# Kernel tuning notes

Hardware: AMD Instinct MI355X
Metric: run time of the kernel (lower is better)

The kernel has to match this reference:

```python
import jax, jax.numpy as jnp
import numpy as np

N, E, D = 50000, 800000, 128
BN_EPS = 1e-5
COORDS_WEIGHT = 1.0


def _p(key, shape, scale=0.05):
    return (jax.random.normal(key, shape, dtype=jnp.float32) * scale)


def setup_inputs() -> dict:
    key = jax.random.key(0)
    ks = jax.random.split(key, 16)
    inp = {
        "h": jax.random.normal(ks[0], (N, D), dtype=jnp.float32),
        "coord": jax.random.normal(ks[1], (N, 3), dtype=jnp.float32),
        "edge_index": jax.random.randint(ks[2], (2, E), 0, N, dtype=jnp.int32),
        # edge_mlp: Linear(2D+1 -> D), BN, ReLU, Linear(D -> D), BN, ReLU
        "e_w1": _p(ks[3], (D, 2 * D + 1)), "e_b1": jnp.zeros((D,), jnp.float32),
        "e_g1": jnp.ones((D,), jnp.float32), "e_be1": jnp.zeros((D,), jnp.float32),
        "e_w2": _p(ks[4], (D, D)), "e_b2": jnp.zeros((D,), jnp.float32),
        "e_g2": jnp.ones((D,), jnp.float32), "e_be2": jnp.zeros((D,), jnp.float32),
        # node_mlp: Linear(D + D -> D), BN, ReLU, Linear(D -> D)
        "n_w1": _p(ks[5], (D, 2 * D)), "n_b1": jnp.zeros((D,), jnp.float32),
        "n_g1": jnp.ones((D,), jnp.float32), "n_be1": jnp.zeros((D,), jnp.float32),
        "n_w2": _p(ks[6], (D, D)), "n_b2": jnp.zeros((D,), jnp.float32),
        # coord_mlp: Linear(D -> D), BN, ReLU, Linear(D -> 1, bias=False, tiny init)
        "c_w1": _p(ks[7], (D, D)), "c_b1": jnp.zeros((D,), jnp.float32),
        "c_g1": jnp.ones((D,), jnp.float32), "c_be1": jnp.zeros((D,), jnp.float32),
        "c_w2": _p(ks[8], (1, D), scale=0.001),
    }
    return inp


def _bn(x, g, b):
    # BatchNorm1d in training mode: biased batch stats over dim 0
    m = jnp.mean(x, axis=0)
    v = jnp.var(x, axis=0)
    return (x - m) * jax.lax.rsqrt(v + BN_EPS) * g + b


def _segment_mean(data, seg, num_segments):
    s = jax.ops.segment_sum(data, seg, num_segments=num_segments)
    c = jax.ops.segment_sum(jnp.ones((data.shape[0], 1), data.dtype), seg,
                            num_segments=num_segments)
    return s / jnp.maximum(c, 1.0)


def reference(h, coord, edge_index,
              e_w1, e_b1, e_g1, e_be1, e_w2, e_b2, e_g2, e_be2,
              n_w1, n_b1, n_g1, n_be1, n_w2, n_b2,
              c_w1, c_b1, c_g1, c_be1, c_w2):
    row, col = edge_index[0], edge_index[1]
    # coord2radial
    coord_diff = coord[row] - coord[col]                      # [E,3]
    radial = jnp.sum(coord_diff ** 2, axis=1, keepdims=True)  # [E,1]
    # edge_model
    e_in = jnp.concatenate([h[row], h[col], radial], axis=1)  # [E, 2D+1]
    x = jax.nn.relu(_bn(e_in @ e_w1.T + e_b1, e_g1, e_be1))
    edge_feat = jax.nn.relu(_bn(x @ e_w2.T + e_b2, e_g2, e_be2))  # [E,D]
    # coord_model
    y = jax.nn.relu(_bn(edge_feat @ c_w1.T + c_b1, c_g1, c_be1))
    scale = y @ c_w2.T                                        # [E,1]
    trans = jnp.clip(coord_diff * scale, -100.0, 100.0)
    coord_out = coord + _segment_mean(trans, row, coord.shape[0]) * COORDS_WEIGHT
    # node_model
    agg = _segment_mean(edge_feat, row, h.shape[0])           # [N,D]
    n_in = jnp.concatenate([h, agg], axis=1)                  # [N,2D]
    z = jax.nn.relu(_bn(n_in @ n_w1.T + n_b1, n_g1, n_be1))
    h_out = h + (z @ n_w2.T + n_b2)                           # recurrent residual
    return (h_out, coord_out)
```

## Files before the change

kernel.cpp:

```cpp
#include <hip/hip_runtime.h>

#define Nn 50000
#define En 800000
#define NSLOT 64

typedef __attribute__((ext_vector_type(8))) short short8;
typedef __attribute__((ext_vector_type(4))) float f32x4;

union U8 { uint4 u4; unsigned short us[8]; short8 s8; };

static __device__ __forceinline__ float bf2f(unsigned int lo16) {
  return __uint_as_float(lo16 << 16);
}
static __device__ __forceinline__ unsigned short f2bf(float f) {
  unsigned int x = __float_as_uint(f);
  return (unsigned short)((x + 0x7FFFu + ((x >> 16) & 1u)) >> 16);
}


__global__ __launch_bounds__(256) void k_prep_h(const float* __restrict__ h,
                                                unsigned short* __restrict__ nodeA) {
  int idx = blockIdx.x * 256 + threadIdx.x;
  if (idx >= Nn * 128) return;
  int n = idx >> 7, k = idx & 127;
  nodeA[(size_t)n * 256 + k] = f2bf(h[idx]);
}

__global__ __launch_bounds__(256) void k_prep_w(const float* __restrict__ src,
                                                unsigned short* __restrict__ dst, int Ksrc,
                                                int koff, int kshift, int total) {
  int idx = blockIdx.x * 256 + threadIdx.x;
  if (idx >= total) return;
  int n = idx >> kshift;
  int k = idx & ((1 << kshift) - 1);
  dst[idx] = f2bf(src[n * Ksrc + koff + k]);
}

__global__ void k_wlast(const float* __restrict__ e_w1, float* __restrict__ wlast) {
  int t = threadIdx.x;
  if (t < 128) wlast[t] = e_w1[t * 257 + 256];
}


__global__ __launch_bounds__(256) void k_count(const int* __restrict__ row, int* __restrict__ cnt) {
  int e = blockIdx.x * 256 + threadIdx.x;
  atomicAdd(&cnt[row[e]], 1);
}

__global__ __launch_bounds__(256) void k_fill(const int* __restrict__ row,
                                              const int* __restrict__ col,
                                              int* __restrict__ cursor,
                                              unsigned short* __restrict__ rowS,
                                              unsigned short* __restrict__ colS) {
  int e = blockIdx.x * 256 + threadIdx.x;
  int r = row[e];
  int pos = atomicAdd(&cursor[r], 1);
  rowS[pos] = (unsigned short)r;
  colS[pos] = (unsigned short)col[e];
}

__global__ __launch_bounds__(1024) void k_scan(const int* __restrict__ cnt, int* __restrict__ start,
                                               int* __restrict__ cursor, int n) {
  __shared__ int wsum[16];
  __shared__ int carry;
  int tid = threadIdx.x, lane = tid & 63, wid = tid >> 6;
  if (tid == 0) carry = 0;
  __syncthreads();
  for (int base = 0; base < n; base += 1024) {
    int i = base + tid;
    int v = (i < n) ? cnt[i] : 0;
    int x = v;
#pragma unroll
    for (int d = 1; d < 64; d <<= 1) {
      int y = __shfl_up(x, d, 64);
      if (lane >= d) x += y;
    }
    if (lane == 63) wsum[wid] = x;
    __syncthreads();
    if (wid == 0) {
      int s = (lane < 16) ? wsum[lane] : 0;
#pragma unroll
      for (int d = 1; d < 16; d <<= 1) {
        int y = __shfl_up(s, d, 64);
        if (lane >= d) s += y;
      }
      if (lane < 16) wsum[lane] = s;
    }
    __syncthreads();
    int c0 = carry;
    int waveoff = (wid > 0) ? wsum[wid - 1] : 0;
    int incl = c0 + waveoff + x;
    if (i < n) {
      start[i] = incl - v;
      cursor[i] = incl - v;
    }
    __syncthreads();
    if (tid == 1023) carry = incl;
    __syncthreads();
  }
}


__global__ void k_fin(const float* __restrict__ statS, const float* __restrict__ statQ,
                      const float* __restrict__ g, const float* __restrict__ be, float invR,
                      float* __restrict__ bnS, float* __restrict__ bnSh) {
  int c = threadIdx.x;
  if (c >= 128) return;
  float s = 0.f, q = 0.f;
  for (int k = 0; k < NSLOT; ++k) {
    s += statS[k * 128 + c];
    q += statQ[k * 128 + c];
  }
  float mean = s * invR;
  float var = fmaxf(q * invR - mean * mean, 0.f);
  float rs = rsqrtf(var + 1e-5f);
  float sc = g[c] * rs;
  bnS[c] = sc;
  bnSh[c] = be[c] - mean * sc;
}

template <int KSTEPS, bool BN_A, bool STATS, bool FP32OUT, bool STORE>
__global__ __launch_bounds__(256) void k_gemmW(
    const unsigned short* __restrict__ A, int Astride,
    const unsigned short* __restrict__ W, const float* __restrict__ bias,
    const float* __restrict__ bnS, const float* __restrict__ bnSh,
    unsigned short* __restrict__ outb, float* __restrict__ statS, float* __restrict__ statQ,
    const float* __restrict__ hres, float* __restrict__ outf, int R) {
  constexpr int K = KSTEPS * 32;
  constexpr int WST = K + 8;
  constexpr int SEGS = K / 8;
  __shared__ __align__(16) unsigned short smem[128 * WST];
  __shared__ float ssum[4][128], ssq[4][128];
  int tid = threadIdx.x;
  int w = tid >> 6, lane = tid & 63, m = lane & 15, kq = lane >> 4;
  int rbase = blockIdx.x * 128;
#pragma unroll
  for (int it = 0; it < SEGS / 2; ++it) {
    int idx = it * 256 + tid;
    int n = idx / SEGS, seg = idx % SEGS;
    uint4 v = *(const uint4*)(W + (size_t)n * K + seg * 8);
    *(uint4*)(smem + n * WST + seg * 8) = v;
  }
  __syncthreads();
  int row0 = rbase + w * 32 + m;
  int rc0 = min(row0, R - 1);
  int rc1 = min(row0 + 16, R - 1);
  f32x4 acc[2][8];
#pragma unroll
  for (int rt = 0; rt < 2; ++rt)
#pragma unroll
    for (int c = 0; c < 8; ++c) acc[rt][c] = (f32x4){0.f, 0.f, 0.f, 0.f};
#pragma unroll
  for (int ks = 0; ks < KSTEPS; ++ks) {
    int k0 = ks * 32 + kq * 8;
    U8 ua0, ua1;
    ua0.u4 = *(const uint4*)(A + (size_t)rc0 * Astride + k0);
    ua1.u4 = *(const uint4*)(A + (size_t)rc1 * Astride + k0);
    if (BN_A) {
      const float4* sp = (const float4*)(bnS + k0);
      const float4* hp = (const float4*)(bnSh + k0);
      float4 s0 = sp[0], s1 = sp[1], h0 = hp[0], h1 = hp[1];
      float sv[8] = {s0.x, s0.y, s0.z, s0.w, s1.x, s1.y, s1.z, s1.w};
      float hv[8] = {h0.x, h0.y, h0.z, h0.w, h1.x, h1.y, h1.z, h1.w};
#pragma unroll
      for (int j = 0; j < 8; ++j) {
        ua0.us[j] = f2bf(fmaxf(bf2f(ua0.us[j]) * sv[j] + hv[j], 0.f));
        ua1.us[j] = f2bf(fmaxf(bf2f(ua1.us[j]) * sv[j] + hv[j], 0.f));
      }
    }
#pragma unroll
    for (int c = 0; c < 8; ++c) {
      U8 ub;
      ub.u4 = *(const uint4*)(smem + (c * 16 + m) * WST + k0);
      acc[0][c] = __builtin_amdgcn_mfma_f32_16x16x32_bf16(ua0.s8, ub.s8, acc[0][c], 0, 0, 0);
      acc[1][c] = __builtin_amdgcn_mfma_f32_16x16x32_bf16(ua1.s8, ub.s8, acc[1][c], 0, 0, 0);
    }
  }
  if constexpr (FP32OUT) {
#pragma unroll
    for (int rt = 0; rt < 2; ++rt)
#pragma unroll
      for (int c = 0; c < 8; ++c) {
        int n = c * 16 + m;
        float bn_ = bias[n];
#pragma unroll
        for (int j = 0; j < 4; ++j) {
          int rr = rbase + w * 32 + rt * 16 + kq * 4 + j;
          if (rr < R) {
            size_t o = (size_t)rr * 128 + n;
            outf[o] = acc[rt][c][j] + bn_ + hres[o];
          }
        }
      }
  } else {
    if constexpr (STORE) __syncthreads();
    unsigned short* tile = smem;
#pragma unroll
    for (int c = 0; c < 8; ++c) {
      int n = c * 16 + m;
      float bn_ = bias ? bias[n] : 0.f;
      float s = 0.f, q = 0.f;
#pragma unroll
      for (int rt = 0; rt < 2; ++rt)
#pragma unroll
        for (int j = 0; j < 4; ++j) {
          int lr = w * 32 + rt * 16 + kq * 4 + j;
          float v = acc[rt][c][j] + bn_;
          if (STORE) tile[lr * 136 + n] = f2bf(v);
          if (STATS) {
            float sv = (rbase + lr < R) ? v : 0.f;
            s += sv;
            q = fmaf(sv, sv, q);
          }
        }
      if (STATS) {
        s += __shfl_xor(s, 16, 64); s += __shfl_xor(s, 32, 64);
        q += __shfl_xor(q, 16, 64); q += __shfl_xor(q, 32, 64);
        if (kq == 0) { ssum[w][n] = s; ssq[w][n] = q; }
      }
    }
    if constexpr (STORE) {
      __syncthreads();
      const uint4* tl = (const uint4*)tile;
#pragma unroll
      for (int u = 0; u < 8; ++u) {
        int idx = u * 256 + tid;
        int rr = idx >> 4, seg = idx & 15;
        if (rbase + rr < R)
          *(uint4*)(outb + (size_t)(rbase + rr) * 128 + seg * 8) = tl[rr * 17 + seg];
      }
    }
    if (STATS) {
      __syncthreads();
      if (tid < 128) {
        float s = ssum[0][tid] + ssum[1][tid] + ssum[2][tid] + ssum[3][tid];
        float q = ssq[0][tid] + ssq[1][tid] + ssq[2][tid] + ssq[3][tid];
        int slot = blockIdx.x & (NSLOT - 1);
        atomicAdd(&statS[slot * 128 + tid], s);
        atomicAdd(&statQ[slot * 128 + tid], q);
      }
    }
  }
}

__global__ __launch_bounds__(256) void k_stats1(
    const unsigned short* __restrict__ hWr, const unsigned short* __restrict__ hWc,
    const float* __restrict__ coord, const unsigned short* __restrict__ rowS,
    const unsigned short* __restrict__ colS, const float* __restrict__ wlast,
    float* __restrict__ radS, float* __restrict__ statS, float* __restrict__ statQ,
    int per_wave) {
  int tid = threadIdx.x, lane = tid & 63;
  int wid = blockIdx.x * 4 + (tid >> 6);
  int e0 = wid * per_wave;
  int e1 = min(e0 + per_wave, En);
  int c2 = lane * 2;
  float wl0 = wlast[c2], wl1 = wlast[c2 + 1];
  float s0 = 0.f, s1 = 0.f, q0 = 0.f, q1 = 0.f;
  for (int e = e0; e < e1; ++e) {
    int r = rowS[e], c = colS[e];
    float dx = coord[r * 3 + 0] - coord[c * 3 + 0];
    float dy = coord[r * 3 + 1] - coord[c * 3 + 1];
    float dz = coord[r * 3 + 2] - coord[c * 3 + 2];
    float rad = dx * dx + dy * dy + dz * dz;
    if (lane == 0) radS[e] = rad;
    unsigned int ua = *(const unsigned int*)(hWr + (size_t)r * 128 + c2);
    unsigned int ub = *(const unsigned int*)(hWc + (size_t)c * 128 + c2);
    float v0 = bf2f(ua & 0xFFFFu) + bf2f(ub & 0xFFFFu) + rad * wl0;
    float v1 = bf2f(ua >> 16) + bf2f(ub >> 16) + rad * wl1;
    s0 += v0; q0 = fmaf(v0, v0, q0);
    s1 += v1; q1 = fmaf(v1, v1, q1);
  }
  int slot = wid & (NSLOT - 1);
  atomicAdd(&statS[slot * 128 + c2], s0);
  atomicAdd(&statS[slot * 128 + c2 + 1], s1);
  atomicAdd(&statQ[slot * 128 + c2], q0);
  atomicAdd(&statQ[slot * 128 + c2 + 1], q1);
}

__global__ __launch_bounds__(256) void k_egemm2(
    const unsigned short* __restrict__ hWr, const unsigned short* __restrict__ hWc,
    const float* __restrict__ radS, const unsigned short* __restrict__ rowS,
    const unsigned short* __restrict__ colS, const unsigned short* __restrict__ W,
    const float* __restrict__ bias, const float* __restrict__ wlast,
    const float* __restrict__ bnS1, const float* __restrict__ bnSh1,
    unsigned short* __restrict__ outb, float* __restrict__ statS, float* __restrict__ statQ) {
  constexpr int WST = 136;
  __shared__ __align__(16) unsigned short smem[128 * WST];
  __shared__ float ssum[4][128], ssq[4][128];
  int tid = threadIdx.x;
  int w = tid >> 6, lane = tid & 63, m = lane & 15, kq = lane >> 4;
  int rbase = blockIdx.x * 128;
#pragma unroll
  for (int it = 0; it < 8; ++it) {
    int idx = it * 256 + tid;
    int n = idx >> 4, seg = idx & 15;
    uint4 v = *(const uint4*)(W + (size_t)n * 128 + seg * 8);
    *(uint4*)(smem + n * WST + seg * 8) = v;
  }
  int rc0 = rbase + w * 32 + m, rc1 = rc0 + 16;
  int r0 = rowS[rc0], c0 = colS[rc0];
  int r1 = rowS[rc1], c1 = colS[rc1];
  float rad0 = radS[rc0], rad1 = radS[rc1];
  __syncthreads();
  f32x4 acc[2][8];
#pragma unroll
  for (int rt = 0; rt < 2; ++rt)
#pragma unroll
    for (int c = 0; c < 8; ++c) acc[rt][c] = (f32x4){0.f, 0.f, 0.f, 0.f};
#pragma unroll
  for (int ks = 0; ks < 4; ++ks) {
    int k0 = ks * 32 + kq * 8;
    U8 a0r, a0c, a1r, a1c;
    a0r.u4 = *(const uint4*)(hWr + (size_t)r0 * 128 + k0);
    a0c.u4 = *(const uint4*)(hWc + (size_t)c0 * 128 + k0);
    a1r.u4 = *(const uint4*)(hWr + (size_t)r1 * 128 + k0);
    a1c.u4 = *(const uint4*)(hWc + (size_t)c1 * 128 + k0);
    const float4* wp = (const float4*)(wlast + k0);
    const float4* sp = (const float4*)(bnS1 + k0);
    const float4* hp = (const float4*)(bnSh1 + k0);
    float4 w0 = wp[0], w1 = wp[1], sA = sp[0], sB = sp[1], hA = hp[0], hB = hp[1];
    float wv[8] = {w0.x, w0.y, w0.z, w0.w, w1.x, w1.y, w1.z, w1.w};
    float sv[8] = {sA.x, sA.y, sA.z, sA.w, sB.x, sB.y, sB.z, sB.w};
    float hv[8] = {hA.x, hA.y, hA.z, hA.w, hB.x, hB.y, hB.z, hB.w};
    U8 ua0, ua1;
#pragma unroll
    for (int j = 0; j < 8; ++j) {
      float v0 = bf2f(a0r.us[j]) + bf2f(a0c.us[j]) + rad0 * wv[j];
      float v1 = bf2f(a1r.us[j]) + bf2f(a1c.us[j]) + rad1 * wv[j];
      ua0.us[j] = f2bf(fmaxf(v0 * sv[j] + hv[j], 0.f));
      ua1.us[j] = f2bf(fmaxf(v1 * sv[j] + hv[j], 0.f));
    }
#pragma unroll
    for (int c = 0; c < 8; ++c) {
      U8 ub;
      ub.u4 = *(const uint4*)(smem + (c * 16 + m) * WST + k0);
      acc[0][c] = __builtin_amdgcn_mfma_f32_16x16x32_bf16(ua0.s8, ub.s8, acc[0][c], 0, 0, 0);
      acc[1][c] = __builtin_amdgcn_mfma_f32_16x16x32_bf16(ua1.s8, ub.s8, acc[1][c], 0, 0, 0);
    }
  }
  __syncthreads();
  unsigned short* tile = smem;
#pragma unroll
  for (int c = 0; c < 8; ++c) {
    int n = c * 16 + m;
    float bn_ = bias[n];
    float s = 0.f, q = 0.f;
#pragma unroll
    for (int rt = 0; rt < 2; ++rt)
#pragma unroll
      for (int j = 0; j < 4; ++j) {
        int lr = w * 32 + rt * 16 + kq * 4 + j;
        float v = acc[rt][c][j] + bn_;
        tile[lr * 136 + n] = f2bf(v);
        s += v;
        q = fmaf(v, v, q);
      }
    s += __shfl_xor(s, 16, 64); s += __shfl_xor(s, 32, 64);
    q += __shfl_xor(q, 16, 64); q += __shfl_xor(q, 32, 64);
    if (kq == 0) { ssum[w][n] = s; ssq[w][n] = q; }
  }
  __syncthreads();
  const uint4* tl = (const uint4*)tile;
#pragma unroll
  for (int u = 0; u < 8; ++u) {
    int idx = u * 256 + tid;
    int rr = idx >> 4, seg = idx & 15;
    *(uint4*)(outb + (size_t)(rbase + rr) * 128 + seg * 8) = tl[rr * 17 + seg];
  }
  if (tid < 128) {
    float s = ssum[0][tid] + ssum[1][tid] + ssum[2][tid] + ssum[3][tid];
    float q = ssq[0][tid] + ssq[1][tid] + ssq[2][tid] + ssq[3][tid];
    int slot = blockIdx.x & (NSLOT - 1);
    atomicAdd(&statS[slot * 128 + tid], s);
    atomicAdd(&statQ[slot * 128 + tid], q);
  }
}

__global__ __launch_bounds__(256) void k_c1agg(
    const unsigned short* __restrict__ t, const unsigned short* __restrict__ W,
    const float* __restrict__ bias, const float* __restrict__ bnS2,
    const float* __restrict__ bnSh2, const float* __restrict__ bnS3,
    const float* __restrict__ bnSh3, const float* __restrict__ cw2,
    const unsigned short* __restrict__ rowS, float* __restrict__ aggAcc,
    float* __restrict__ scaleE) {
  __shared__ __align__(16) unsigned short smw[128 * 128];
  __shared__ __align__(16) unsigned short ytile[128 * 128];
  int tid = threadIdx.x;
  int w = tid >> 6, lane = tid & 63, m = lane & 15, kq = lane >> 4;
  int rbase = blockIdx.x * 128;
#pragma unroll
  for (int it = 0; it < 8; ++it) {
    int idx = it * 256 + tid;
    int n = idx >> 4, b = idx & 15;
    uint4 v = *(const uint4*)(W + (size_t)n * 128 + b * 8);
    *(uint4*)(smw + n * 128 + ((b ^ (n & 15)) << 3)) = v;
  }
  __syncthreads();
  f32x4 acc[2][8];
#pragma unroll
  for (int rt = 0; rt < 2; ++rt)
#pragma unroll
    for (int c = 0; c < 8; ++c) acc[rt][c] = (f32x4){0.f, 0.f, 0.f, 0.f};
  int r0l = w * 32 + m, r1l = r0l + 16;
#pragma unroll
  for (int ks = 0; ks < 4; ++ks) {
    int k0 = ks * 32 + kq * 8;
    int blk = ks * 4 + kq;
    U8 ua0, ua1;
    ua0.u4 = *(const uint4*)(t + (size_t)(rbase + r0l) * 128 + k0);
    ua1.u4 = *(const uint4*)(t + (size_t)(rbase + r1l) * 128 + k0);
    const float4* sp = (const float4*)(bnS2 + k0);
    const float4* hp = (const float4*)(bnSh2 + k0);
    float4 sA = sp[0], sB = sp[1], hA = hp[0], hB = hp[1];
    float sv[8] = {sA.x, sA.y, sA.z, sA.w, sB.x, sB.y, sB.z, sB.w};
    float hv[8] = {hA.x, hA.y, hA.z, hA.w, hB.x, hB.y, hB.z, hB.w};
#pragma unroll
    for (int j = 0; j < 8; ++j) {
      ua0.us[j] = f2bf(fmaxf(bf2f(ua0.us[j]) * sv[j] + hv[j], 0.f));
      ua1.us[j] = f2bf(fmaxf(bf2f(ua1.us[j]) * sv[j] + hv[j], 0.f));
    }
    *(uint4*)(ytile + r0l * 128 + ((blk ^ m) << 3)) = ua0.u4;
    *(uint4*)(ytile + r1l * 128 + ((blk ^ m) << 3)) = ua1.u4;
#pragma unroll
    for (int c = 0; c < 8; ++c) {
      U8 ub;
      ub.u4 = *(const uint4*)(smw + (c * 16 + m) * 128 + ((blk ^ m) << 3));
      acc[0][c] = __builtin_amdgcn_mfma_f32_16x16x32_bf16(ua0.s8, ub.s8, acc[0][c], 0, 0, 0);
      acc[1][c] = __builtin_amdgcn_mfma_f32_16x16x32_bf16(ua1.s8, ub.s8, acc[1][c], 0, 0, 0);
    }
  }
  float p[2][4] = {{0.f, 0.f, 0.f, 0.f}, {0.f, 0.f, 0.f, 0.f}};
#pragma unroll
  for (int c = 0; c < 8; ++c) {
    int n = c * 16 + m;
    float b1 = bias[n], s3 = bnS3[n], sh3 = bnSh3[n], w2 = cw2[n];
#pragma unroll
    for (int rt = 0; rt < 2; ++rt)
#pragma unroll
      for (int j = 0; j < 4; ++j) {
        float t3v = acc[rt][c][j] + b1;
        p[rt][j] += w2 * fmaxf(t3v * s3 + sh3, 0.f);
      }
  }
#pragma unroll
  for (int rt = 0; rt < 2; ++rt)
#pragma unroll
    for (int j = 0; j < 4; ++j) {
      float v = p[rt][j];
      v += __shfl_xor(v, 1, 64); v += __shfl_xor(v, 2, 64);
      v += __shfl_xor(v, 4, 64); v += __shfl_xor(v, 8, 64);
      if (m == 0) scaleE[rbase + w * 32 + rt * 16 + kq * 4 + j] = v;
    }
  __syncthreads();
  int ch = tid & 127, half = tid >> 7;
  int rlo = half * 64, rhi = rlo + 64;
  int cur = rowS[rbase + rlo];
  float run = 0.f;
  for (int r = rlo; r < rhi; ++r) {
    int nid = rowS[rbase + r];
    if (nid != cur) {
      atomicAdd(&aggAcc[(size_t)cur * 128 + ch], run);
      run = 0.f;
      cur = nid;
    }
    run += bf2f(ytile[r * 128 + (((ch >> 3) ^ (r & 15)) << 3) + (ch & 7)]);
  }
  atomicAdd(&aggAcc[(size_t)cur * 128 + ch], run);
}

__global__ __launch_bounds__(256) void k_aggfin(const float* __restrict__ aggAcc,
                                                const int* __restrict__ cnt,
                                                unsigned short* __restrict__ nodeA) {
  int idx = blockIdx.x * 256 + threadIdx.x;
  if (idx >= Nn * 128) return;
  int n = idx >> 7, ch = idx & 127;
  float inv = 1.f / fmaxf((float)cnt[n], 1.f);
  nodeA[(size_t)n * 256 + 128 + ch] = f2bf(aggAcc[idx] * inv);
}

__global__ __launch_bounds__(256) void k_coord(const float* __restrict__ coord,
                                               const unsigned short* __restrict__ colS,
                                               const int* __restrict__ start,
                                               const int* __restrict__ cnt,
                                               const float* __restrict__ scaleE,
                                               float* __restrict__ cout) {
  int tid = threadIdx.x;
  int lane = tid & 63;
  int n = blockIdx.x * 4 + (tid >> 6);
  if (n >= Nn) return;
  int deg = cnt[n], off = start[n];
  float cx0 = coord[n * 3 + 0], cy0 = coord[n * 3 + 1], cz0 = coord[n * 3 + 2];
  float ax = 0.f, ay = 0.f, az = 0.f;
  for (int j = lane; j < deg; j += 64) {
    int e = off + j;
    int c = colS[e];
    float s = scaleE[e];
    float tx = (cx0 - coord[c * 3 + 0]) * s;
    float ty = (cy0 - coord[c * 3 + 1]) * s;
    float tz = (cz0 - coord[c * 3 + 2]) * s;
    ax += fminf(fmaxf(tx, -100.f), 100.f);
    ay += fminf(fmaxf(ty, -100.f), 100.f);
    az += fminf(fmaxf(tz, -100.f), 100.f);
  }
#pragma unroll
  for (int d = 32; d; d >>= 1) {
    ax += __shfl_xor(ax, d, 64);
    ay += __shfl_xor(ay, d, 64);
    az += __shfl_xor(az, d, 64);
  }
  if (lane == 0) {
    float inv = 1.f / fmaxf((float)deg, 1.f);
    cout[n * 3 + 0] = cx0 + ax * inv;
    cout[n * 3 + 1] = cy0 + ay * inv;
    cout[n * 3 + 2] = cz0 + az * inv;
  }
}


extern "C" void kernel_launch(void* const* d_in, const int* in_sizes, int n_in, void* d_out,
                              int out_size, void* d_ws, size_t ws_size, hipStream_t stream) {
  (void)in_sizes; (void)n_in; (void)out_size; (void)ws_size;
  const float* h = (const float*)d_in[0];
  const float* coord = (const float*)d_in[1];
  const int* eidx = (const int*)d_in[2];
  const int* row = eidx;
  const int* col = eidx + En;
  const float* e_w1 = (const float*)d_in[3];
  const float* e_b1 = (const float*)d_in[4];
  const float* e_g1 = (const float*)d_in[5];
  const float* e_be1 = (const float*)d_in[6];
  const float* e_w2 = (const float*)d_in[7];
  const float* e_b2 = (const float*)d_in[8];
  const float* e_g2 = (const float*)d_in[9];
  const float* e_be2 = (const float*)d_in[10];
  const float* n_w1 = (const float*)d_in[11];
  const float* n_b1 = (const float*)d_in[12];
  const float* n_g1 = (const float*)d_in[13];
  const float* n_be1 = (const float*)d_in[14];
  const float* n_w2 = (const float*)d_in[15];
  const float* n_b2 = (const float*)d_in[16];
  const float* c_w1 = (const float*)d_in[17];
  const float* c_b1 = (const float*)d_in[18];
  const float* c_g1 = (const float*)d_in[19];
  const float* c_be1 = (const float*)d_in[20];
  const float* c_w2 = (const float*)d_in[21];

  char* base = (char*)d_ws;
  size_t off = 0;
  auto alloc = [&](size_t bytes) -> void* {
    void* p = base + off;
    off = (off + bytes + 255) & ~(size_t)255;
    return p;
  };
  unsigned short* t = (unsigned short*)alloc((size_t)En * 128 * 2);
  unsigned short* nodeA = (unsigned short*)alloc((size_t)Nn * 256 * 2);
  unsigned short* hWr = (unsigned short*)alloc((size_t)Nn * 128 * 2);
  unsigned short* hWc = (unsigned short*)alloc((size_t)Nn * 128 * 2);
  float* aggAcc = (float*)hWr;
  float* scaleE = (float*)alloc((size_t)En * 4);
  float* radS = scaleE;
  unsigned short* rowS = (unsigned short*)alloc((size_t)En * 2);
  unsigned short* colS = (unsigned short*)alloc((size_t)En * 2);
  int* cnt = (int*)alloc((size_t)Nn * 4);
  int* startp = (int*)alloc((size_t)Nn * 4);
  int* cursor = (int*)alloc((size_t)Nn * 4);
  float* statS = (float*)alloc(4 * NSLOT * 128 * 4);
  float* statQ = (float*)alloc(4 * NSLOT * 128 * 4);
  float* bnS = (float*)alloc(4 * 128 * 4);
  float* bnSh = (float*)alloc(4 * 128 * 4);
  unsigned short* w1a = (unsigned short*)alloc(128 * 128 * 2);
  unsigned short* w1b = (unsigned short*)alloc(128 * 128 * 2);
  unsigned short* w2b = (unsigned short*)alloc(128 * 128 * 2);
  unsigned short* c1b = (unsigned short*)alloc(128 * 128 * 2);
  unsigned short* n1b = (unsigned short*)alloc(128 * 256 * 2);
  unsigned short* n2b = (unsigned short*)alloc(128 * 128 * 2);
  float* wlast = (float*)alloc(128 * 4);

  hipMemsetAsync(cnt, 0, (size_t)Nn * 4, stream);
  hipMemsetAsync(statS, 0, 4 * NSLOT * 128 * 4, stream);
  hipMemsetAsync(statQ, 0, 4 * NSLOT * 128 * 4, stream);

  k_prep_h<<<(Nn * 128 + 255) / 256, 256, 0, stream>>>(h, nodeA);
  k_prep_w<<<(128 * 128 + 255) / 256, 256, 0, stream>>>(e_w1, w1a, 257, 0, 7, 128 * 128);
  k_prep_w<<<(128 * 128 + 255) / 256, 256, 0, stream>>>(e_w1, w1b, 257, 128, 7, 128 * 128);
  k_prep_w<<<(128 * 128 + 255) / 256, 256, 0, stream>>>(e_w2, w2b, 128, 0, 7, 128 * 128);
  k_prep_w<<<(128 * 128 + 255) / 256, 256, 0, stream>>>(c_w1, c1b, 128, 0, 7, 128 * 128);
  k_prep_w<<<(128 * 256 + 255) / 256, 256, 0, stream>>>(n_w1, n1b, 256, 0, 8, 128 * 256);
  k_prep_w<<<(128 * 128 + 255) / 256, 256, 0, stream>>>(n_w2, n2b, 128, 0, 7, 128 * 128);
  k_wlast<<<1, 128, 0, stream>>>(e_w1, wlast);

  k_count<<<En / 256, 256, 0, stream>>>(row, cnt);
  k_scan<<<1, 1024, 0, stream>>>(cnt, startp, cursor, Nn);
  k_fill<<<En / 256, 256, 0, stream>>>(row, col, cursor, rowS, colS);

  const int gridN = (Nn + 127) / 128;
  k_gemmW<4, false, false, false, true><<<gridN, 256, 0, stream>>>(
      nodeA, 256, w1a, e_b1, nullptr, nullptr, hWr, nullptr, nullptr, nullptr, nullptr, Nn);
  k_gemmW<4, false, false, false, true><<<gridN, 256, 0, stream>>>(
      nodeA, 256, w1b, nullptr, nullptr, nullptr, hWc, nullptr, nullptr, nullptr, nullptr, Nn);

  const int per_wave = (En + 5119) / 5120;
  k_stats1<<<1280, 256, 0, stream>>>(hWr, hWc, coord, rowS, colS, wlast, radS,
                                     statS + 0 * NSLOT * 128, statQ + 0 * NSLOT * 128, per_wave);
  k_fin<<<1, 128, 0, stream>>>(statS + 0 * NSLOT * 128, statQ + 0 * NSLOT * 128, e_g1, e_be1,
                               1.f / En, bnS + 0, bnSh + 0);

  k_egemm2<<<En / 128, 256, 0, stream>>>(hWr, hWc, radS, rowS, colS, w2b, e_b2, wlast, bnS + 0,
                                         bnSh + 0, t, statS + 1 * NSLOT * 128,
                                         statQ + 1 * NSLOT * 128);
  k_fin<<<1, 128, 0, stream>>>(statS + 1 * NSLOT * 128, statQ + 1 * NSLOT * 128, e_g2, e_be2,
                               1.f / En, bnS + 128, bnSh + 128);

  hipMemsetAsync(aggAcc, 0, (size_t)Nn * 128 * 4, stream);

  k_gemmW<4, true, true, false, false><<<En / 128, 256, 0, stream>>>(
      t, 128, c1b, c_b1, bnS + 128, bnSh + 128, nullptr, statS + 2 * NSLOT * 128,
      statQ + 2 * NSLOT * 128, nullptr, nullptr, En);
  k_fin<<<1, 128, 0, stream>>>(statS + 2 * NSLOT * 128, statQ + 2 * NSLOT * 128, c_g1, c_be1,
                               1.f / En, bnS + 256, bnSh + 256);

  k_c1agg<<<En / 128, 256, 0, stream>>>(t, c1b, c_b1, bnS + 128, bnSh + 128, bnS + 256,
                                        bnSh + 256, c_w2, rowS, aggAcc, scaleE);
  k_aggfin<<<(Nn * 128 + 255) / 256, 256, 0, stream>>>(aggAcc, cnt, nodeA);

  float* hout = (float*)d_out;
  float* cout = hout + (size_t)Nn * 128;
  k_coord<<<(Nn + 3) / 4, 256, 0, stream>>>(coord, colS, startp, cnt, scaleE, cout);

  k_gemmW<8, false, true, false, true><<<gridN, 256, 0, stream>>>(
      nodeA, 256, n1b, n_b1, nullptr, nullptr, t, statS + 3 * NSLOT * 128,
      statQ + 3 * NSLOT * 128, nullptr, nullptr, Nn);
  k_fin<<<1, 128, 0, stream>>>(statS + 3 * NSLOT * 128, statQ + 3 * NSLOT * 128, n_g1, n_be1,
                               1.f / Nn, bnS + 384, bnSh + 384);
  k_gemmW<4, true, false, true, true><<<gridN, 256, 0, stream>>>(
      t, 128, n2b, n_b2, bnS + 384, bnSh + 384, nullptr, nullptr, nullptr, h, hout, Nn);
}
```

Baseline: 958.3 us.

## Move edge aggregation into coord stats pass and slim the scale kernel

Segment-sum aggregation of edge features now runs in the first coord-MLP pass, which also computes BN statistics, replacing the generic stats GEMM with a dedicated fused kernel. The aggregation works from the activated tile kept in registers and reuses the same LDS buffer for the weights. The second pass now only computes the per-edge scale. It drops the aggregation and uses a padded-stride LDS layout instead of an XOR swizzle, halving its shared memory and possibly raising occupancy. The stats kernel now uses a single 32KB LDS buffer plus extra syncs and holds the activations in registers, which raises register pressure.

```diff
diff --git a/kernel.cpp b/kernel.cpp
--- a/kernel.cpp
+++ b/kernel.cpp
@@ -376,36 +376,134 @@
   }
 }
 
-__global__ __launch_bounds__(256) void k_c1agg(
+__global__ __launch_bounds__(256) void k_caggstats(
+    const unsigned short* __restrict__ t, const unsigned short* __restrict__ W,
+    const float* __restrict__ bias, const float* __restrict__ bnS2,
+    const float* __restrict__ bnSh2, const unsigned short* __restrict__ rowS,
+    float* __restrict__ aggAcc, float* __restrict__ statS, float* __restrict__ statQ) {
+  __shared__ __align__(16) unsigned short yb[128 * 128];
+  __shared__ float ssum[4][128], ssq[4][128];
+  int tid = threadIdx.x;
+  int w = tid >> 6, lane = tid & 63, m = lane & 15, kq = lane >> 4;
+  int rbase = blockIdx.x * 128;
+  int r0l = w * 32 + m, r1l = r0l + 16;
+  U8 ya0[4], ya1[4];
+#pragma unroll
+  for (int ks = 0; ks < 4; ++ks) {
+    int k0 = ks * 32 + kq * 8;
+    int blk = ks * 4 + kq;
+    ya0[ks].u4 = *(const uint4*)(t + (size_t)(rbase + r0l) * 128 + k0);
+    ya1[ks].u4 = *(const uint4*)(t + (size_t)(rbase + r1l) * 128 + k0);
+    const float4* sp = (const float4*)(bnS2 + k0);
+    const float4* hp = (const float4*)(bnSh2 + k0);
+    float4 sA = sp[0], sB = sp[1], hA = hp[0], hB = hp[1];
+    float sv[8] = {sA.x, sA.y, sA.z, sA.w, sB.x, sB.y, sB.z, sB.w};
+    float hv[8] = {hA.x, hA.y, hA.z, hA.w, hB.x, hB.y, hB.z, hB.w};
+#pragma unroll
+    for (int j = 0; j < 8; ++j) {
+      ya0[ks].us[j] = f2bf(fmaxf(bf2f(ya0[ks].us[j]) * sv[j] + hv[j], 0.f));
+      ya1[ks].us[j] = f2bf(fmaxf(bf2f(ya1[ks].us[j]) * sv[j] + hv[j], 0.f));
+    }
+    *(uint4*)(yb + r0l * 128 + ((blk ^ m) << 3)) = ya0[ks].u4;
+    *(uint4*)(yb + r1l * 128 + ((blk ^ m) << 3)) = ya1[ks].u4;
+  }
+  __syncthreads();
+  {
+    int ch = tid & 127, half = tid >> 7;
+    int rlo = half * 64, rhi = rlo + 64;
+    int cur = rowS[rbase + rlo];
+    float run = 0.f;
+    for (int r = rlo; r < rhi; ++r) {
+      int nid = rowS[rbase + r];
+      if (nid != cur) {
+        atomicAdd(&aggAcc[(size_t)cur * 128 + ch], run);
+        run = 0.f;
+        cur = nid;
+      }
+      run += bf2f(yb[r * 128 + (((ch >> 3) ^ (r & 15)) << 3) + (ch & 7)]);
+    }
+    atomicAdd(&aggAcc[(size_t)cur * 128 + ch], run);
+  }
+  __syncthreads();
+#pragma unroll
+  for (int it = 0; it < 8; ++it) {
+    int idx = it * 256 + tid;
+    int n = idx >> 4, b = idx & 15;
+    uint4 v = *(const uint4*)(W + (size_t)n * 128 + b * 8);
+    *(uint4*)(yb + n * 128 + ((b ^ (n & 15)) << 3)) = v;
+  }
+  __syncthreads();
+  f32x4 acc[2][8];
+#pragma unroll
+  for (int rt = 0; rt < 2; ++rt)
+#pragma unroll
+    for (int c = 0; c < 8; ++c) acc[rt][c] = (f32x4){0.f, 0.f, 0.f, 0.f};
+#pragma unroll
+  for (int ks = 0; ks < 4; ++ks) {
+    int blk = ks * 4 + kq;
+#pragma unroll
+    for (int c = 0; c < 8; ++c) {
+      U8 ub;
+      ub.u4 = *(const uint4*)(yb + (c * 16 + m) * 128 + ((blk ^ m) << 3));
+      acc[0][c] = __builtin_amdgcn_mfma_f32_16x16x32_bf16(ya0[ks].s8, ub.s8, acc[0][c], 0, 0, 0);
+      acc[1][c] = __builtin_amdgcn_mfma_f32_16x16x32_bf16(ya1[ks].s8, ub.s8, acc[1][c], 0, 0, 0);
+    }
+  }
+#pragma unroll
+  for (int c = 0; c < 8; ++c) {
+    int n = c * 16 + m;
+    float bn_ = bias[n];
+    float s = 0.f, q = 0.f;
+#pragma unroll
+    for (int rt = 0; rt < 2; ++rt)
+#pragma unroll
+      for (int j = 0; j < 4; ++j) {
+        float v = acc[rt][c][j] + bn_;
+        s += v;
+        q = fmaf(v, v, q);
+      }
+    s += __shfl_xor(s, 16, 64); s += __shfl_xor(s, 32, 64);
+    q += __shfl_xor(q, 16, 64); q += __shfl_xor(q, 32, 64);
+    if (kq == 0) { ssum[w][n] = s; ssq[w][n] = q; }
+  }
+  __syncthreads();
+  if (tid < 128) {
+    float s = ssum[0][tid] + ssum[1][tid] + ssum[2][tid] + ssum[3][tid];
+    float q = ssq[0][tid] + ssq[1][tid] + ssq[2][tid] + ssq[3][tid];
+    int slot = blockIdx.x & (NSLOT - 1);
+    atomicAdd(&statS[slot * 128 + tid], s);
+    atomicAdd(&statQ[slot * 128 + tid], q);
+  }
+}
+
+__global__ __launch_bounds__(256) void k_cscale(
     const unsigned short* __restrict__ t, const unsigned short* __restrict__ W,
     const float* __restrict__ bias, const float* __restrict__ bnS2,
     const float* __restrict__ bnSh2, const float* __restrict__ bnS3,
     const float* __restrict__ bnSh3, const float* __restrict__ cw2,
-    const unsigned short* __restrict__ rowS, float* __restrict__ aggAcc,
     float* __restrict__ scaleE) {
-  __shared__ __align__(16) unsigned short smw[128 * 128];
-  __shared__ __align__(16) unsigned short ytile[128 * 128];
+  constexpr int WST = 136;
+  __shared__ __align__(16) unsigned short smem[128 * WST];
   int tid = threadIdx.x;
   int w = tid >> 6, lane = tid & 63, m = lane & 15, kq = lane >> 4;
   int rbase = blockIdx.x * 128;
 #pragma unroll
   for (int it = 0; it < 8; ++it) {
     int idx = it * 256 + tid;
-    int n = idx >> 4, b = idx & 15;
-    uint4 v = *(const uint4*)(W + (size_t)n * 128 + b * 8);
-    *(uint4*)(smw + n * 128 + ((b ^ (n & 15)) << 3)) = v;
-  }
-  __syncthreads();
+    int n = idx >> 4, seg = idx & 15;
+    uint4 v = *(const uint4*)(W + (size_t)n * 128 + seg * 8);
+    *(uint4*)(smem + n * WST + seg * 8) = v;
+  }
+  __syncthreads();
+  int r0l = w * 32 + m, r1l = r0l + 16;
   f32x4 acc[2][8];
 #pragma unroll
   for (int rt = 0; rt < 2; ++rt)
 #pragma unroll
     for (int c = 0; c < 8; ++c) acc[rt][c] = (f32x4){0.f, 0.f, 0.f, 0.f};
-  int r0l = w * 32 + m, r1l = r0l + 16;
 #pragma unroll
   for (int ks = 0; ks < 4; ++ks) {
     int k0 = ks * 32 + kq * 8;
-    int blk = ks * 4 + kq;
     U8 ua0, ua1;
     ua0.u4 = *(const uint4*)(t + (size_t)(rbase + r0l) * 128 + k0);
     ua1.u4 = *(const uint4*)(t + (size_t)(rbase + r1l) * 128 + k0);
@@ -419,12 +517,10 @@
       ua0.us[j] = f2bf(fmaxf(bf2f(ua0.us[j]) * sv[j] + hv[j], 0.f));
       ua1.us[j] = f2bf(fmaxf(bf2f(ua1.us[j]) * sv[j] + hv[j], 0.f));
     }
-    *(uint4*)(ytile + r0l * 128 + ((blk ^ m) << 3)) = ua0.u4;
-    *(uint4*)(ytile + r1l * 128 + ((blk ^ m) << 3)) = ua1.u4;
 #pragma unroll
     for (int c = 0; c < 8; ++c) {
       U8 ub;
-      ub.u4 = *(const uint4*)(smw + (c * 16 + m) * 128 + ((blk ^ m) << 3));
+      ub.u4 = *(const uint4*)(smem + (c * 16 + m) * WST + k0);
       acc[0][c] = __builtin_amdgcn_mfma_f32_16x16x32_bf16(ua0.s8, ub.s8, acc[0][c], 0, 0, 0);
       acc[1][c] = __builtin_amdgcn_mfma_f32_16x16x32_bf16(ua1.s8, ub.s8, acc[1][c], 0, 0, 0);
     }
@@ -451,21 +547,6 @@
       v += __shfl_xor(v, 4, 64); v += __shfl_xor(v, 8, 64);
       if (m == 0) scaleE[rbase + w * 32 + rt * 16 + kq * 4 + j] = v;
     }
-  __syncthreads();
-  int ch = tid & 127, half = tid >> 7;
-  int rlo = half * 64, rhi = rlo + 64;
-  int cur = rowS[rbase + rlo];
-  float run = 0.f;
-  for (int r = rlo; r < rhi; ++r) {
-    int nid = rowS[rbase + r];
-    if (nid != cur) {
-      atomicAdd(&aggAcc[(size_t)cur * 128 + ch], run);
-      run = 0.f;
-      cur = nid;
-    }
-    run += bf2f(ytile[r * 128 + (((ch >> 3) ^ (r & 15)) << 3) + (ch & 7)]);
-  }
-  atomicAdd(&aggAcc[(size_t)cur * 128 + ch], run);
 }
 
 __global__ __launch_bounds__(256) void k_aggfin(const float* __restrict__ aggAcc,
@@ -613,14 +694,13 @@
 
   hipMemsetAsync(aggAcc, 0, (size_t)Nn * 128 * 4, stream);
 
-  k_gemmW<4, true, true, false, false><<<En / 128, 256, 0, stream>>>(
-      t, 128, c1b, c_b1, bnS + 128, bnSh + 128, nullptr, statS + 2 * NSLOT * 128,
-      statQ + 2 * NSLOT * 128, nullptr, nullptr, En);
+  k_caggstats<<<En / 128, 256, 0, stream>>>(t, c1b, c_b1, bnS + 128, bnSh + 128, rowS, aggAcc,
+                                            statS + 2 * NSLOT * 128, statQ + 2 * NSLOT * 128);
   k_fin<<<1, 128, 0, stream>>>(statS + 2 * NSLOT * 128, statQ + 2 * NSLOT * 128, c_g1, c_be1,
                                1.f / En, bnS + 256, bnSh + 256);
 
-  k_c1agg<<<En / 128, 256, 0, stream>>>(t, c1b, c_b1, bnS + 128, bnSh + 128, bnS + 256,
-                                        bnSh + 256, c_w2, rowS, aggAcc, scaleE);
+  k_cscale<<<En / 128, 256, 0, stream>>>(t, c1b, c_b1, bnS + 128, bnSh + 128, bnS + 256,
+                                         bnSh + 256, c_w2, scaleE);
   k_aggfin<<<(Nn * 128 + 255) / 256, 256, 0, stream>>>(aggAcc, cnt, nodeA);
 
   float* hout = (float*)d_out;
```

New measurement: 973.5 us. Within noise of the previous version (+1.6%).

## Replace second coord GEMM with stored output and CSR-based per-node aggregation

Applied to the files above, without the earlier changes.

The coord-MLP first GEMM now writes its pre-BN output in place over t, so the scale computation becomes a cheap per-edge reduction kernel instead of redoing the 128x128 GEMM. Node aggregation is rewritten as a per-node gather over the sorted CSR edge ranges, with one wave per node, and runs before t is overwritten. This drops the fp32 atomic accumulation buffer, its memset and the finalize kernel. The stats kernel also processes two edges per iteration to expose more memory-level parallelism, which assumes each wave's edge span is even.

```diff
diff --git a/kernel.cpp b/kernel.cpp
--- a/kernel.cpp
+++ b/kernel.cpp
@@ -256,19 +256,33 @@
   int c2 = lane * 2;
   float wl0 = wlast[c2], wl1 = wlast[c2 + 1];
   float s0 = 0.f, s1 = 0.f, q0 = 0.f, q1 = 0.f;
-  for (int e = e0; e < e1; ++e) {
-    int r = rowS[e], c = colS[e];
-    float dx = coord[r * 3 + 0] - coord[c * 3 + 0];
-    float dy = coord[r * 3 + 1] - coord[c * 3 + 1];
-    float dz = coord[r * 3 + 2] - coord[c * 3 + 2];
-    float rad = dx * dx + dy * dy + dz * dz;
-    if (lane == 0) radS[e] = rad;
-    unsigned int ua = *(const unsigned int*)(hWr + (size_t)r * 128 + c2);
-    unsigned int ub = *(const unsigned int*)(hWc + (size_t)c * 128 + c2);
-    float v0 = bf2f(ua & 0xFFFFu) + bf2f(ub & 0xFFFFu) + rad * wl0;
-    float v1 = bf2f(ua >> 16) + bf2f(ub >> 16) + rad * wl1;
-    s0 += v0; q0 = fmaf(v0, v0, q0);
-    s1 += v1; q1 = fmaf(v1, v1, q1);
+  for (int e = e0; e < e1; e += 2) {
+    int ra = rowS[e], ca = colS[e];
+    int rb = rowS[e + 1], cb = colS[e + 1];
+    float ax = coord[ra * 3 + 0] - coord[ca * 3 + 0];
+    float ay = coord[ra * 3 + 1] - coord[ca * 3 + 1];
+    float az = coord[ra * 3 + 2] - coord[ca * 3 + 2];
+    float bx = coord[rb * 3 + 0] - coord[cb * 3 + 0];
+    float by = coord[rb * 3 + 1] - coord[cb * 3 + 1];
+    float bz = coord[rb * 3 + 2] - coord[cb * 3 + 2];
+    float rada = ax * ax + ay * ay + az * az;
+    float radb = bx * bx + by * by + bz * bz;
+    if (lane == 0) {
+      radS[e] = rada;
+      radS[e + 1] = radb;
+    }
+    unsigned int uar = *(const unsigned int*)(hWr + (size_t)ra * 128 + c2);
+    unsigned int uac = *(const unsigned int*)(hWc + (size_t)ca * 128 + c2);
+    unsigned int ubr = *(const unsigned int*)(hWr + (size_t)rb * 128 + c2);
+    unsigned int ubc = *(const unsigned int*)(hWc + (size_t)cb * 128 + c2);
+    float va0 = bf2f(uar & 0xFFFFu) + bf2f(uac & 0xFFFFu) + rada * wl0;
+    float va1 = bf2f(uar >> 16) + bf2f(uac >> 16) + rada * wl1;
+    float vb0 = bf2f(ubr & 0xFFFFu) + bf2f(ubc & 0xFFFFu) + radb * wl0;
+    float vb1 = bf2f(ubr >> 16) + bf2f(ubc >> 16) + radb * wl1;
+    s0 += va0 + vb0;
+    s1 += va1 + vb1;
+    q0 = fmaf(va0, va0, q0); q0 = fmaf(vb0, vb0, q0);
+    q1 = fmaf(va1, va1, q1); q1 = fmaf(vb1, vb1, q1);
   }
   int slot = wid & (NSLOT - 1);
   atomicAdd(&statS[slot * 128 + c2], s0);
@@ -376,106 +390,57 @@
   }
 }
 
-__global__ __launch_bounds__(256) void k_c1agg(
-    const unsigned short* __restrict__ t, const unsigned short* __restrict__ W,
-    const float* __restrict__ bias, const float* __restrict__ bnS2,
-    const float* __restrict__ bnSh2, const float* __restrict__ bnS3,
-    const float* __restrict__ bnSh3, const float* __restrict__ cw2,
-    const unsigned short* __restrict__ rowS, float* __restrict__ aggAcc,
-    float* __restrict__ scaleE) {
-  __shared__ __align__(16) unsigned short smw[128 * 128];
-  __shared__ __align__(16) unsigned short ytile[128 * 128];
+__global__ __launch_bounds__(256) void k_agg(const unsigned short* __restrict__ t,
+                                             const int* __restrict__ start,
+                                             const int* __restrict__ cnt,
+                                             const float* __restrict__ bnS,
+                                             const float* __restrict__ bnSh,
+                                             unsigned short* __restrict__ nodeA) {
   int tid = threadIdx.x;
-  int w = tid >> 6, lane = tid & 63, m = lane & 15, kq = lane >> 4;
-  int rbase = blockIdx.x * 128;
-#pragma unroll
-  for (int it = 0; it < 8; ++it) {
-    int idx = it * 256 + tid;
-    int n = idx >> 4, b = idx & 15;
-    uint4 v = *(const uint4*)(W + (size_t)n * 128 + b * 8);
-    *(uint4*)(smw + n * 128 + ((b ^ (n & 15)) << 3)) = v;
-  }
-  __syncthreads();
-  f32x4 acc[2][8];
-#pragma unroll
-  for (int rt = 0; rt < 2; ++rt)
-#pragma unroll
-    for (int c = 0; c < 8; ++c) acc[rt][c] = (f32x4){0.f, 0.f, 0.f, 0.f};
-  int r0l = w * 32 + m, r1l = r0l + 16;
-#pragma unroll
-  for (int ks = 0; ks < 4; ++ks) {
-    int k0 = ks * 32 + kq * 8;
-    int blk = ks * 4 + kq;
-    U8 ua0, ua1;
-    ua0.u4 = *(const uint4*)(t + (size_t)(rbase + r0l) * 128 + k0);
-    ua1.u4 = *(const uint4*)(t + (size_t)(rbase + r1l) * 128 + k0);
-    const float4* sp = (const float4*)(bnS2 + k0);
-    const float4* hp = (const float4*)(bnSh2 + k0);
-    float4 sA = sp[0], sB = sp[1], hA = hp[0], hB = hp[1];
-    float sv[8] = {sA.x, sA.y, sA.z, sA.w, sB.x, sB.y, sB.z, sB.w};
-    float hv[8] = {hA.x, hA.y, hA.z, hA.w, hB.x, hB.y, hB.z, hB.w};
-#pragma unroll
-    for (int j = 0; j < 8; ++j) {
-      ua0.us[j] = f2bf(fmaxf(bf2f(ua0.us[j]) * sv[j] + hv[j], 0.f));
-      ua1.us[j] = f2bf(fmaxf(bf2f(ua1.us[j]) * sv[j] + hv[j], 0.f));
-    }
-    *(uint4*)(ytile + r0l * 128 + ((blk ^ m) << 3)) = ua0.u4;
-    *(uint4*)(ytile + r1l * 128 + ((blk ^ m) << 3)) = ua1.u4;
-#pragma unroll
-    for (int c = 0; c < 8; ++c) {
-      U8 ub;
-      ub.u4 = *(const uint4*)(smw + (c * 16 + m) * 128 + ((blk ^ m) << 3));
-      acc[0][c] = __builtin_amdgcn_mfma_f32_16x16x32_bf16(ua0.s8, ub.s8, acc[0][c], 0, 0, 0);
-      acc[1][c] = __builtin_amdgcn_mfma_f32_16x16x32_bf16(ua1.s8, ub.s8, acc[1][c], 0, 0, 0);
-    }
-  }
-  float p[2][4] = {{0.f, 0.f, 0.f, 0.f}, {0.f, 0.f, 0.f, 0.f}};
-#pragma unroll
-  for (int c = 0; c < 8; ++c) {
-    int n = c * 16 + m;
-    float b1 = bias[n], s3 = bnS3[n], sh3 = bnSh3[n], w2 = cw2[n];
-#pragma unroll
-    for (int rt = 0; rt < 2; ++rt)
-#pragma unroll
-      for (int j = 0; j < 4; ++j) {
-        float t3v = acc[rt][c][j] + b1;
-        p[rt][j] += w2 * fmaxf(t3v * s3 + sh3, 0.f);
-      }
-  }
-#pragma unroll
-  for (int rt = 0; rt < 2; ++rt)
-#pragma unroll
-    for (int j = 0; j < 4; ++j) {
-      float v = p[rt][j];
-      v += __shfl_xor(v, 1, 64); v += __shfl_xor(v, 2, 64);
-      v += __shfl_xor(v, 4, 64); v += __shfl_xor(v, 8, 64);
-      if (m == 0) scaleE[rbase + w * 32 + rt * 16 + kq * 4 + j] = v;
-    }
-  __syncthreads();
-  int ch = tid & 127, half = tid >> 7;
-  int rlo = half * 64, rhi = rlo + 64;
-  int cur = rowS[rbase + rlo];
-  float run = 0.f;
-  for (int r = rlo; r < rhi; ++r) {
-    int nid = rowS[rbase + r];
-    if (nid != cur) {
-      atomicAdd(&aggAcc[(size_t)cur * 128 + ch], run);
-      run = 0.f;
-      cur = nid;
-    }
-    run += bf2f(ytile[r * 128 + (((ch >> 3) ^ (r & 15)) << 3) + (ch & 7)]);
-  }
-  atomicAdd(&aggAcc[(size_t)cur * 128 + ch], run);
-}
-
-__global__ __launch_bounds__(256) void k_aggfin(const float* __restrict__ aggAcc,
-                                                const int* __restrict__ cnt,
-                                                unsigned short* __restrict__ nodeA) {
-  int idx = blockIdx.x * 256 + threadIdx.x;
-  if (idx >= Nn * 128) return;
-  int n = idx >> 7, ch = idx & 127;
-  float inv = 1.f / fmaxf((float)cnt[n], 1.f);
-  nodeA[(size_t)n * 256 + 128 + ch] = f2bf(aggAcc[idx] * inv);
+  int lane = tid & 63;
+  int n = blockIdx.x * 4 + (tid >> 6);
+  if (n >= Nn) return;
+  int deg = cnt[n], off = start[n];
+  int c2 = lane * 2;
+  float s0 = bnS[c2], s1 = bnS[c2 + 1], h0 = bnSh[c2], h1 = bnSh[c2 + 1];
+  float a0 = 0.f, a1 = 0.f;
+  const unsigned short* p = t + (size_t)off * 128 + c2;
+  for (int j = 0; j < deg; ++j) {
+    unsigned int u = *(const unsigned int*)(p + (size_t)j * 128);
+    a0 += fmaxf(bf2f(u & 0xFFFFu) * s0 + h0, 0.f);
+    a1 += fmaxf(bf2f(u >> 16) * s1 + h1, 0.f);
+  }
+  float inv = 1.f / fmaxf((float)deg, 1.f);
+  unsigned int o = (unsigned)f2bf(a0 * inv) | ((unsigned)f2bf(a1 * inv) << 16);
+  *(unsigned int*)(nodeA + (size_t)n * 256 + 128 + c2) = o;
+}
+
+__global__ __launch_bounds__(256) void k_scale2(const unsigned short* __restrict__ t,
+                                                const float* __restrict__ bnS3,
+                                                const float* __restrict__ bnSh3,
+                                                const float* __restrict__ cw2,
+                                                float* __restrict__ scaleE) {
+  int tid = threadIdx.x, lane = tid & 63, w = tid >> 6;
+  long e = (long)blockIdx.x * 8 + w * 2;
+  int c2 = lane * 2;
+  float s0 = bnS3[c2], s1 = bnS3[c2 + 1];
+  float h0 = bnSh3[c2], h1 = bnSh3[c2 + 1];
+  float w0 = cw2[c2], w1 = cw2[c2 + 1];
+  unsigned int ua = *(const unsigned int*)(t + e * 128 + c2);
+  unsigned int ub = *(const unsigned int*)(t + (e + 1) * 128 + c2);
+  float pa = fmaxf(bf2f(ua & 0xFFFFu) * s0 + h0, 0.f) * w0 +
+             fmaxf(bf2f(ua >> 16) * s1 + h1, 0.f) * w1;
+  float pb = fmaxf(bf2f(ub & 0xFFFFu) * s0 + h0, 0.f) * w0 +
+             fmaxf(bf2f(ub >> 16) * s1 + h1, 0.f) * w1;
+#pragma unroll
+  for (int d = 32; d; d >>= 1) {
+    pa += __shfl_xor(pa, d, 64);
+    pb += __shfl_xor(pb, d, 64);
+  }
+  if (lane == 0) {
+    scaleE[e] = pa;
+    scaleE[e + 1] = pb;
+  }
 }
 
 __global__ __launch_bounds__(256) void k_coord(const float* __restrict__ coord,
@@ -556,7 +521,6 @@
   unsigned short* nodeA = (unsigned short*)alloc((size_t)Nn * 256 * 2);
   unsigned short* hWr = (unsigned short*)alloc((size_t)Nn * 128 * 2);
   unsigned short* hWc = (unsigned short*)alloc((size_t)Nn * 128 * 2);
-  float* aggAcc = (float*)hWr;
   float* scaleE = (float*)alloc((size_t)En * 4);
   float* radS = scaleE;
   unsigned short* rowS = (unsigned short*)alloc((size_t)En * 2);
@@ -599,7 +563,7 @@
   k_gemmW<4, false, false, false, true><<<gridN, 256, 0, stream>>>(
       nodeA, 256, w1b, nullptr, nullptr, nullptr, hWc, nullptr, nullptr, nullptr, nullptr, Nn);
 
-  const int per_wave = (En + 5119) / 5120;
+  const int per_wave = ((En / 2 + 5119) / 5120) * 2;
   k_stats1<<<1280, 256, 0, stream>>>(hWr, hWc, coord, rowS, colS, wlast, radS,
                                      statS + 0 * NSLOT * 128, statQ + 0 * NSLOT * 128, per_wave);
   k_fin<<<1, 128, 0, stream>>>(statS + 0 * NSLOT * 128, statQ + 0 * NSLOT * 128, e_g1, e_be1,
@@ -611,17 +575,15 @@
   k_fin<<<1, 128, 0, stream>>>(statS + 1 * NSLOT * 128, statQ + 1 * NSLOT * 128, e_g2, e_be2,
                                1.f / En, bnS + 128, bnSh + 128);
 
-  hipMemsetAsync(aggAcc, 0, (size_t)Nn * 128 * 4, stream);
-
-  k_gemmW<4, true, true, false, false><<<En / 128, 256, 0, stream>>>(
-      t, 128, c1b, c_b1, bnS + 128, bnSh + 128, nullptr, statS + 2 * NSLOT * 128,
+  k_agg<<<(Nn + 3) / 4, 256, 0, stream>>>(t, startp, cnt, bnS + 128, bnSh + 128, nodeA);
+
+  k_gemmW<4, true, true, false, true><<<En / 128, 256, 0, stream>>>(
+      t, 128, c1b, c_b1, bnS + 128, bnSh + 128, t, statS + 2 * NSLOT * 128,
       statQ + 2 * NSLOT * 128, nullptr, nullptr, En);
   k_fin<<<1, 128, 0, stream>>>(statS + 2 * NSLOT * 128, statQ + 2 * NSLOT * 128, c_g1, c_be1,
                                1.f / En, bnS + 256, bnSh + 256);
 
-  k_c1agg<<<En / 128, 256, 0, stream>>>(t, c1b, c_b1, bnS + 128, bnSh + 128, bnS + 256,
-                                        bnSh + 256, c_w2, rowS, aggAcc, scaleE);
-  k_aggfin<<<(Nn * 128 + 255) / 256, 256, 0, stream>>>(aggAcc, cnt, nodeA);
+  k_scale2<<<En / 8, 256, 0, stream>>>(t, bnS + 256, bnSh + 256, c_w2, scaleE);
 
   float* hout = (float*)d_out;
   float* cout = hout + (size_t)Nn * 128;
```

Result: faster. 794.4 us (-17.1%).
